# Performance work log

Measured on AMD Instinct MI355X. Metric: run time of the kernel, lower is better.

The kernel has to match this reference:

```python
import jax, jax.numpy as jnp
import numpy as np

B, T, N = 8, 128, 512
HID = 4              # hidden_channels (GAT out, heads=1)
IN = 1               # in_channels (forced by unsqueeze(-1))
D = N * HID          # LSTM input == hidden size = 2048
E = 16384            # num edges (avg degree 32)
OUT = N              # out_channels
NEG_SLOPE = 0.2      # PyG GATConv default


def setup_inputs() -> dict:
    key = jax.random.key(0)
    ks = jax.random.split(key, 12)
    inv = 1.0 / np.sqrt(D)
    return {
        "x_sequence": jax.random.normal(ks[0], (B, T, N), jnp.float32),
        "gat_w": jax.random.normal(ks[1], (HID, IN), jnp.float32),
        "att_src": jax.random.normal(ks[2], (HID,), jnp.float32) * 0.5,
        "att_dst": jax.random.normal(ks[3], (HID,), jnp.float32) * 0.5,
        "gat_bias": jnp.zeros((HID,), jnp.float32),
        "w_ih": jax.random.normal(ks[4], (4 * D, D), jnp.float32) * inv,
        "w_hh": jax.random.normal(ks[5], (4 * D, D), jnp.float32) * inv,
        "b_ih": jnp.zeros((4 * D,), jnp.float32),
        "b_hh": jnp.zeros((4 * D,), jnp.float32),
        "w_lin": jax.random.normal(ks[6], (OUT, D), jnp.float32) * inv,
        "b_lin": jnp.zeros((OUT,), jnp.float32),
        "edge_index": jax.random.randint(ks[7], (2, E), 0, N, jnp.int32),
    }


def _gat(x_flat, src, dst, W, a_s, a_d, bias):
    # x_flat: [BN, 1]; PyG GATConv heads=1, eval mode (dropout off)
    BN = B * N
    h = x_flat @ W.T                                   # [BN, HID]
    e = jax.nn.leaky_relu((h @ a_s)[src] + (h @ a_d)[dst], NEG_SLOPE)
    m = jax.ops.segment_max(e, dst, num_segments=BN)   # every node has a self-loop
    ex = jnp.exp(e - m[dst])
    denom = jax.ops.segment_sum(ex, dst, num_segments=BN)
    alpha = ex / denom[dst]
    out = jax.ops.segment_sum(alpha[:, None] * h[src], dst, num_segments=BN)
    return out + bias


def reference(x_sequence, gat_w, att_src, att_dst, gat_bias,
              w_ih, w_hh, b_ih, b_hh, w_lin, b_lin, edge_index):
    BN = B * N
    # add self-loops over all B*N flattened nodes (PyG add_self_loops=True);
    # original edge_index only touches nodes < N -- faithfully reproduced.
    loops = jnp.arange(BN, dtype=edge_index.dtype)
    src = jnp.concatenate([edge_index[0], loops])
    dst = jnp.concatenate([edge_index[1], loops])

    # batch the per-timestep GAT: [T, B*N, 1]
    xt = x_sequence.transpose(1, 0, 2).reshape(T, BN, IN)
    g = jax.vmap(lambda x: jax.nn.relu(
        _gat(x, src, dst, gat_w, att_src, att_dst, gat_bias)))(xt)  # [T, BN, HID]
    seq = g.reshape(T, B, D)                           # [T, B, N*HID]

    def step(carry, x_t):
        h, c = carry
        z = x_t @ w_ih.T + h @ w_hh.T + (b_ih + b_hh)  # [B, 4D]
        i, f, gg, o = jnp.split(z, 4, axis=-1)         # torch gate order i,f,g,o
        c = jax.nn.sigmoid(f) * c + jax.nn.sigmoid(i) * jnp.tanh(gg)
        h = jax.nn.sigmoid(o) * jnp.tanh(c)
        return (h, c), None

    h0 = jnp.zeros((B, D), x_sequence.dtype)
    (hT, _), _ = jax.lax.scan(step, (h0, h0), seq)     # hT == lstm_out[:, -1, :]
    return hT @ w_lin.T + b_lin                        # [B, OUT]
```

## Files before the change

kernel.cpp:

```cpp
#include <hip/hip_runtime.h>
#include <hip/hip_cooperative_groups.h>
#include <math.h>

#define BB 8
#define TT 128
#define NN 512
#define HH 4
#define DD 2048
#define EE 16384
#define KTOT 4096
#define NKB 128
#define XROW 4112
#define FPAD 16

typedef __attribute__((ext_vector_type(8))) short short8;
typedef __attribute__((ext_vector_type(4))) float f32x4;

__device__ __forceinline__ float b2f(unsigned short u) {
    union { unsigned int i; float f; } v; v.i = ((unsigned int)u) << 16; return v.f;
}
__device__ __forceinline__ unsigned short f2b(float f) {
    union { float f; unsigned int i; } v; v.f = f;
    unsigned int r = v.i + 0x7fff + ((v.i >> 16) & 1);
    return (unsigned short)(r >> 16);
}


__global__ void k_csr_zero(int* __restrict__ counts, int* __restrict__ fill) {
    int i = threadIdx.x;
    counts[i] = 0;
    fill[i] = 0;
}

__global__ void k_csr_count(const int* __restrict__ ei, int* __restrict__ counts) {
    int e = blockIdx.x * blockDim.x + threadIdx.x;
    if (e < EE) atomicAdd(&counts[ei[EE + e]], 1);
}

__global__ void k_csr_scan(const int* __restrict__ counts, int* __restrict__ offs) {
    int s = 0;
    for (int i = 0; i < NN; ++i) { offs[i] = s; s += counts[i]; }
    offs[NN] = s;
}

__global__ void k_csr_fill(const int* __restrict__ ei, const int* __restrict__ offs,
                           int* __restrict__ fill, int* __restrict__ csr_src) {
    int e = blockIdx.x * blockDim.x + threadIdx.x;
    if (e < EE) {
        int d = ei[EE + e];
        int pos = atomicAdd(&fill[d], 1);
        csr_src[offs[d] + pos] = ei[e];
    }
}


__global__ void k_gat0(const float* __restrict__ xseq, const float* __restrict__ W,
                       const float* __restrict__ as, const float* __restrict__ ad,
                       const float* __restrict__ bias, const int* __restrict__ offs,
                       const int* __restrict__ csr_src, unsigned short* __restrict__ seqout) {
    __shared__ float xr[NN];
    const int t = blockIdx.x;
    const int j = threadIdx.x;
    xr[j] = xseq[t * NN + j];
    __syncthreads();

    const float w0 = W[0], w1 = W[1], w2 = W[2], w3 = W[3];
    const float cs = w0 * as[0] + w1 * as[1] + w2 * as[2] + w3 * as[3];
    const float cd = w0 * ad[0] + w1 * ad[1] + w2 * ad[2] + w3 * ad[3];

    const float xj = xr[j];
    const float ed = cd * xj;
    float e0 = (cs + cd) * xj;
    e0 = e0 > 0.f ? e0 : 0.2f * e0;

    const int s0 = offs[j], s1 = offs[j + 1];
    float m = e0;
    for (int p = s0; p < s1; ++p) {
        float e = cs * xr[csr_src[p]] + ed;
        e = e > 0.f ? e : 0.2f * e;
        m = fmaxf(m, e);
    }
    float den = expf(e0 - m);
    float num = den * xj;
    for (int p = s0; p < s1; ++p) {
        int s = csr_src[p];
        float e = cs * xr[s] + ed;
        e = e > 0.f ? e : 0.2f * e;
        float wgt = expf(e - m);
        den += wgt;
        num += wgt * xr[s];
    }
    const float y = num / den;

    ushort4 o;
    o.x = f2b(fmaxf(w0 * y + bias[0], 0.f));
    o.y = f2b(fmaxf(w1 * y + bias[1], 0.f));
    o.z = f2b(fmaxf(w2 * y + bias[2], 0.f));
    o.w = f2b(fmaxf(w3 * y + bias[3], 0.f));
    *(ushort4*)(seqout + (size_t)t * BB * DD + (size_t)j * HH) = o;
}

__global__ void k_gat_rest(const float* __restrict__ xseq, const float* __restrict__ W,
                           const float* __restrict__ bias, unsigned short* __restrict__ seqout) {
    int n = blockIdx.x * blockDim.x + threadIdx.x;
    int t = n / (7 * NN);
    int rem = n - t * (7 * NN);
    int b = 1 + rem / NN;
    int j = rem - (b - 1) * NN;
    float x = xseq[((size_t)b * TT + t) * NN + j];
    const float w0 = W[0], w1 = W[1], w2 = W[2], w3 = W[3];
    ushort4 o;
    o.x = f2b(fmaxf(w0 * x + bias[0], 0.f));
    o.y = f2b(fmaxf(w1 * x + bias[1], 0.f));
    o.z = f2b(fmaxf(w2 * x + bias[2], 0.f));
    o.w = f2b(fmaxf(w3 * x + bias[3], 0.f));
    *(ushort4*)(seqout + (size_t)t * BB * DD + (size_t)b * DD + (size_t)j * HH) = o;
}

__global__ __launch_bounds__(256) void k_pack_w(const float* __restrict__ wih,
                                                const float* __restrict__ whh,
                                                unsigned short* __restrict__ WP) {
    const int pair = blockIdx.x * 4 + (threadIdx.x >> 6);
    const int lane = threadIdx.x & 63;
    const int s = pair >> 7, kb = pair & 127;
    const int n = lane >> 2, quad = lane & 3;
    const int d = (s >> 1) * 8 + (s & 1) * 4 + (n & 3);
    const int row = (n >> 2) * 2048 + d;
    const int k = kb * 32 + quad * 8;
    const float* src = (k < 2048) ? (wih + (size_t)row * 2048 + k)
                                  : (whh + (size_t)row * 2048 + (k - 2048));
    unsigned int u[4];
#pragma unroll
    for (int p = 0; p < 4; ++p)
        u[p] = (unsigned int)f2b(src[2 * p]) | ((unsigned int)f2b(src[2 * p + 1]) << 16);
    ((uint4*)WP)[(size_t)pair * 64 + quad * 16 + n] = make_uint4(u[0], u[1], u[2], u[3]);
}


__global__ void k_zero(unsigned int* __restrict__ hb, unsigned int* __restrict__ bar) {
    int i = blockIdx.x * blockDim.x + threadIdx.x;
    if (i < 16384) hb[i] = 0u;
    if (i < 256 * FPAD) bar[i] = 0u;
}

__global__ __launch_bounds__(1024, 4) void k_lstm_persist(
    const unsigned short* __restrict__ seq, const uint4* __restrict__ WPq,
    const float* __restrict__ b_ih, const float* __restrict__ b_hh,
    unsigned short* __restrict__ hb0, unsigned short* __restrict__ hb1,
    unsigned int* __restrict__ flags) {
    __shared__ unsigned short xh[8][XROW];
    __shared__ float red[2][8][32][4];
    __shared__ float zbuf[4][8][8];
    __shared__ float biasL[32];

    const int tid = threadIdx.x;
    const int wave = tid >> 6, lane = tid & 63;
    const int st = wave >> 3, ke = wave & 7;
    const int d0 = blockIdx.x * 8;
    const size_t sglob = (size_t)blockIdx.x * 2 + st;

    if (tid < 32) {
        const int g = tid >> 3, dl = tid & 7;
        const int row = g * 2048 + d0 + dl;
        biasL[tid] = b_ih[row] + b_hh[row];
    }

    uint4 w[16];
    {
        const uint4* wp = WPq + (sglob * NKB + (size_t)ke * 16) * 64 + lane;
#pragma unroll
        for (int i = 0; i < 16; ++i) w[i] = wp[i * 64];
    }

    const unsigned short* arow = &xh[lane & 7][(lane >> 4) << 3];

    float creg0 = 0.f, creg1 = 0.f;

    for (int t = 0; t < TT; ++t) {
        const unsigned short* xt = seq + (size_t)t * BB * DD;
        const unsigned short* hin = (t & 1) ? hb1 : hb0;
        unsigned short* hout = (t & 1) ? hb0 : hb1;

#pragma unroll
        for (int i = 0; i < 2; ++i) {
            const int c = tid + 1024 * i;
            const int batch = c >> 8;
            const int k = (c & 255) << 3;
            *(uint4*)&xh[batch][k] = *(const uint4*)(xt + batch * DD + k);
        }

        if (t > 0 && tid < 256) {
            const unsigned int gen = (unsigned int)t;
            while (__hip_atomic_load(&flags[tid * FPAD], __ATOMIC_RELAXED,
                                     __HIP_MEMORY_SCOPE_AGENT) < gen) {}
        }
        __syncthreads();

        const unsigned int* hw = (const unsigned int*)hin;
#pragma unroll
        for (int i = 0; i < 8; ++i) {
            const int widx = tid + 1024 * i;
            const int batch = widx >> 10;
            const int dw = widx & 1023;
            unsigned int v = __hip_atomic_load(&hw[widx], __ATOMIC_RELAXED,
                                               __HIP_MEMORY_SCOPE_AGENT);
            ((unsigned int*)&xh[batch][2048])[dw] = v;
        }
        __syncthreads();

        f32x4 acc = {0.f, 0.f, 0.f, 0.f};
#pragma unroll
        for (int i = 0; i < 16; ++i) {
            const int kb = ke * 16 + i;
            short8 a = *(const short8*)(arow + (kb << 5));
            short8 b;
            __builtin_memcpy(&b, &w[i], 16);
            acc = __builtin_amdgcn_mfma_f32_16x16x32_bf16(a, b, acc, 0, 0, 0);
        }
        if (lane < 32) *(f32x4*)&red[st][ke][lane][0] = acc;
        __syncthreads();

        if (tid < 256) {
            const int st2 = tid >> 7, l2 = (tid & 127) >> 2, reg = tid & 3;
            float z = 0.f;
#pragma unroll
            for (int kk = 0; kk < 8; ++kk) z += red[st2][kk][l2][reg];
            const int batch = (l2 >> 4) * 4 + reg;
            const int n = l2 & 15;
            zbuf[n >> 2][st2 * 4 + (n & 3)][batch] = z;
        }
        __syncthreads();

        if (tid < 32) {
            const int batch = tid >> 2, dp = (tid & 3) << 1;
            float h2[2];
#pragma unroll
            for (int q = 0; q < 2; ++q) {
                const int dl = dp + q;
                const float zi = zbuf[0][dl][batch] + biasL[dl];
                const float zf = zbuf[1][dl][batch] + biasL[8 + dl];
                const float zg = zbuf[2][dl][batch] + biasL[16 + dl];
                const float zo = zbuf[3][dl][batch] + biasL[24 + dl];
                const float si = 1.f / (1.f + expf(-zi));
                const float sf = 1.f / (1.f + expf(-zf));
                const float so = 1.f / (1.f + expf(-zo));
                const float tg = tanhf(zg);
                float& cr = q ? creg1 : creg0;
                cr = sf * cr + si * tg;
                h2[q] = so * tanhf(cr);
            }
            const unsigned int pk = (unsigned int)f2b(h2[0]) |
                                    ((unsigned int)f2b(h2[1]) << 16);
            unsigned int* hp = (unsigned int*)(hout + batch * DD + d0) + (tid & 3);
            __hip_atomic_store(hp, pk, __ATOMIC_RELAXED, __HIP_MEMORY_SCOPE_AGENT);
        }
        if (t != TT - 1) {
            __builtin_amdgcn_s_waitcnt(0);
            if (tid == 0)
                __hip_atomic_store(&flags[blockIdx.x * FPAD], (unsigned int)(t + 1),
                                   __ATOMIC_RELAXED, __HIP_MEMORY_SCOPE_AGENT);
        }
    }
}

__global__ void k_final(const unsigned short* __restrict__ h, const float* __restrict__ w_lin,
                        const float* __restrict__ b_lin, float* __restrict__ out) {
    const int wave = threadIdx.x >> 6;
    const int lane = threadIdx.x & 63;
    const int o = blockIdx.x * 4 + wave;
    const float4* w4 = (const float4*)(w_lin + (size_t)o * DD);

    float acc[8];
#pragma unroll
    for (int b = 0; b < 8; ++b) acc[b] = 0.f;
#pragma unroll 2
    for (int it = 0; it < 8; ++it) {
        const int k4 = it * 64 + lane;
        float4 wv = w4[k4];
#pragma unroll
        for (int b = 0; b < 8; ++b) {
            ushort4 hv = *(const ushort4*)(h + (size_t)b * DD + 4 * (size_t)k4);
            acc[b] += wv.x * b2f(hv.x) + wv.y * b2f(hv.y) +
                      wv.z * b2f(hv.z) + wv.w * b2f(hv.w);
        }
    }
#pragma unroll
    for (int b = 0; b < 8; ++b) {
        float v = acc[b];
        v += __shfl_xor(v, 32, 64);
        v += __shfl_xor(v, 16, 64);
        v += __shfl_xor(v, 8, 64);
        v += __shfl_xor(v, 4, 64);
        v += __shfl_xor(v, 2, 64);
        v += __shfl_xor(v, 1, 64);
        acc[b] = v;
    }
    if (lane < 8) out[(size_t)lane * NN + o] = acc[lane] + b_lin[o];
}


extern "C" void kernel_launch(void* const* d_in, const int* in_sizes, int n_in,
                              void* d_out, int out_size, void* d_ws, size_t ws_size,
                              hipStream_t stream) {
    const float* xseq  = (const float*)d_in[0];
    const float* gat_w = (const float*)d_in[1];
    const float* a_src = (const float*)d_in[2];
    const float* a_dst = (const float*)d_in[3];
    const float* g_b   = (const float*)d_in[4];
    const float* w_ih  = (const float*)d_in[5];
    const float* w_hh  = (const float*)d_in[6];
    const float* b_ih  = (const float*)d_in[7];
    const float* b_hh  = (const float*)d_in[8];
    const float* w_lin = (const float*)d_in[9];
    const float* b_lin = (const float*)d_in[10];
    const int*   eidx  = (const int*)d_in[11];
    float* out = (float*)d_out;

    unsigned short* seq = (unsigned short*)d_ws;
    unsigned short* WP  = seq + (size_t)TT * BB * DD;
    unsigned short* hb0 = WP + (size_t)8192 * KTOT;
    unsigned short* hb1 = hb0 + BB * DD;
    unsigned int* flags = (unsigned int*)(hb1 + BB * DD);
    int* counts  = (int*)(flags + 256 * FPAD);
    int* offs    = counts + NN;
    int* fill    = offs + NN + 1;
    int* csr_src = fill + NN;

    k_csr_zero<<<1, NN, 0, stream>>>(counts, fill);
    k_csr_count<<<EE / 256, 256, 0, stream>>>(eidx, counts);
    k_csr_scan<<<1, 1, 0, stream>>>(counts, offs);
    k_csr_fill<<<EE / 256, 256, 0, stream>>>(eidx, offs, fill, csr_src);

    k_pack_w<<<16384, 256, 0, stream>>>(w_ih, w_hh, WP);

    k_gat0<<<TT, NN, 0, stream>>>(xseq, gat_w, a_src, a_dst, g_b, offs, csr_src, seq);
    k_gat_rest<<<(TT * 7 * NN) / 256, 256, 0, stream>>>(xseq, gat_w, g_b, seq);

    k_zero<<<64, 256, 0, stream>>>((unsigned int*)hb0, flags);

    {
        void* kargs[] = {
            (void*)&seq, (void*)&WP, (void*)&b_ih, (void*)&b_hh,
            (void*)&hb0, (void*)&hb1, (void*)&flags,
        };
        hipLaunchCooperativeKernel((const void*)k_lstm_persist, dim3(256), dim3(1024),
                                   kargs, 0, stream);
    }

    k_final<<<NN / 4, 256, 0, stream>>>(hb0, w_lin, b_lin, out);
}
```

Measured before the change: 964.5 us.

## Fuse GAT into one atomic-scatter kernel and load LSTM operands straight to registers

The CSR build kernels and the two GAT kernels are replaced by one kernel per timestep. It scatters edge softmax numerators and denominators with shared-memory atomics and skips the max subtraction, then writes all batches. In the persistent LSTM kernel the x and h operands are now loaded directly from global memory into registers instead of being staged in LDS. The x-part MFMAs are issued before the flag wait, which removes a barrier and lets input work overlap the cross-block sync. The weight packer also switches to float4 loads. Dropping the max subtraction risks overflow in expf for large logits.

```diff
diff --git a/kernel.cpp b/kernel.cpp
--- a/kernel.cpp
+++ b/kernel.cpp
@@ -1,16 +1,13 @@
 #include <hip/hip_runtime.h>
-#include <hip/hip_cooperative_groups.h>
 #include <math.h>
 
 #define BB 8
 #define TT 128
 #define NN 512
-#define HH 4
 #define DD 2048
 #define EE 16384
 #define KTOT 4096
 #define NKB 128
-#define XROW 4112
 #define FPAD 16
 
 typedef __attribute__((ext_vector_type(8))) short short8;
@@ -25,96 +22,60 @@
     return (unsigned short)(r >> 16);
 }
 
-
-__global__ void k_csr_zero(int* __restrict__ counts, int* __restrict__ fill) {
-    int i = threadIdx.x;
-    counts[i] = 0;
-    fill[i] = 0;
-}
-
-__global__ void k_csr_count(const int* __restrict__ ei, int* __restrict__ counts) {
-    int e = blockIdx.x * blockDim.x + threadIdx.x;
-    if (e < EE) atomicAdd(&counts[ei[EE + e]], 1);
-}
-
-__global__ void k_csr_scan(const int* __restrict__ counts, int* __restrict__ offs) {
-    int s = 0;
-    for (int i = 0; i < NN; ++i) { offs[i] = s; s += counts[i]; }
-    offs[NN] = s;
-}
-
-__global__ void k_csr_fill(const int* __restrict__ ei, const int* __restrict__ offs,
-                           int* __restrict__ fill, int* __restrict__ csr_src) {
-    int e = blockIdx.x * blockDim.x + threadIdx.x;
-    if (e < EE) {
-        int d = ei[EE + e];
-        int pos = atomicAdd(&fill[d], 1);
-        csr_src[offs[d] + pos] = ei[e];
-    }
-}
-
-
-__global__ void k_gat0(const float* __restrict__ xseq, const float* __restrict__ W,
-                       const float* __restrict__ as, const float* __restrict__ ad,
-                       const float* __restrict__ bias, const int* __restrict__ offs,
-                       const int* __restrict__ csr_src, unsigned short* __restrict__ seqout) {
-    __shared__ float xr[NN];
+__global__ __launch_bounds__(512) void k_gat(const float* __restrict__ xseq,
+                                             const float* __restrict__ W,
+                                             const float* __restrict__ as,
+                                             const float* __restrict__ ad,
+                                             const float* __restrict__ bias,
+                                             const int* __restrict__ ei,
+                                             unsigned short* __restrict__ seqout) {
+    __shared__ float xr[NN], num[NN], den[NN];
     const int t = blockIdx.x;
     const int j = threadIdx.x;
     xr[j] = xseq[t * NN + j];
-    __syncthreads();
+    num[j] = 0.f;
+    den[j] = 0.f;
 
     const float w0 = W[0], w1 = W[1], w2 = W[2], w3 = W[3];
     const float cs = w0 * as[0] + w1 * as[1] + w2 * as[2] + w3 * as[3];
     const float cd = w0 * ad[0] + w1 * ad[1] + w2 * ad[2] + w3 * ad[3];
-
-    const float xj = xr[j];
-    const float ed = cd * xj;
-    float e0 = (cs + cd) * xj;
-    e0 = e0 > 0.f ? e0 : 0.2f * e0;
-
-    const int s0 = offs[j], s1 = offs[j + 1];
-    float m = e0;
-    for (int p = s0; p < s1; ++p) {
-        float e = cs * xr[csr_src[p]] + ed;
-        e = e > 0.f ? e : 0.2f * e;
-        m = fmaxf(m, e);
-    }
-    float den = expf(e0 - m);
-    float num = den * xj;
-    for (int p = s0; p < s1; ++p) {
-        int s = csr_src[p];
-        float e = cs * xr[s] + ed;
-        e = e > 0.f ? e : 0.2f * e;
-        float wgt = expf(e - m);
-        den += wgt;
-        num += wgt * xr[s];
-    }
-    const float y = num / den;
-
-    ushort4 o;
-    o.x = f2b(fmaxf(w0 * y + bias[0], 0.f));
-    o.y = f2b(fmaxf(w1 * y + bias[1], 0.f));
-    o.z = f2b(fmaxf(w2 * y + bias[2], 0.f));
-    o.w = f2b(fmaxf(w3 * y + bias[3], 0.f));
-    *(ushort4*)(seqout + (size_t)t * BB * DD + (size_t)j * HH) = o;
-}
-
-__global__ void k_gat_rest(const float* __restrict__ xseq, const float* __restrict__ W,
-                           const float* __restrict__ bias, unsigned short* __restrict__ seqout) {
-    int n = blockIdx.x * blockDim.x + threadIdx.x;
-    int t = n / (7 * NN);
-    int rem = n - t * (7 * NN);
-    int b = 1 + rem / NN;
-    int j = rem - (b - 1) * NN;
-    float x = xseq[((size_t)b * TT + t) * NN + j];
-    const float w0 = W[0], w1 = W[1], w2 = W[2], w3 = W[3];
-    ushort4 o;
-    o.x = f2b(fmaxf(w0 * x + bias[0], 0.f));
-    o.y = f2b(fmaxf(w1 * x + bias[1], 0.f));
-    o.z = f2b(fmaxf(w2 * x + bias[2], 0.f));
-    o.w = f2b(fmaxf(w3 * x + bias[3], 0.f));
-    *(ushort4*)(seqout + (size_t)t * BB * DD + (size_t)b * DD + (size_t)j * HH) = o;
+    __syncthreads();
+
+    for (int e = j; e < EE; e += NN) {
+        const int s = ei[e], d = ei[EE + e];
+        float v = cs * xr[s] + cd * xr[d];
+        v = v > 0.f ? v : 0.2f * v;
+        const float wt = expf(v);
+        atomicAdd(&den[d], wt);
+        atomicAdd(&num[d], wt * xr[s]);
+    }
+    __syncthreads();
+
+    const float b0 = bias[0], b1 = bias[1], b2 = bias[2], b3 = bias[3];
+
+    {
+        const float xj = xr[j];
+        float e0 = (cs + cd) * xj;
+        e0 = e0 > 0.f ? e0 : 0.2f * e0;
+        const float we = expf(e0);
+        const float y = (num[j] + we * xj) / (den[j] + we);
+        ushort4 o;
+        o.x = f2b(fmaxf(w0 * y + b0, 0.f));
+        o.y = f2b(fmaxf(w1 * y + b1, 0.f));
+        o.z = f2b(fmaxf(w2 * y + b2, 0.f));
+        o.w = f2b(fmaxf(w3 * y + b3, 0.f));
+        *(ushort4*)(seqout + (size_t)t * BB * DD + (size_t)j * 4) = o;
+    }
+#pragma unroll
+    for (int b = 1; b < 8; ++b) {
+        const float x = xseq[((size_t)b * TT + t) * NN + j];
+        ushort4 o;
+        o.x = f2b(fmaxf(w0 * x + b0, 0.f));
+        o.y = f2b(fmaxf(w1 * x + b1, 0.f));
+        o.z = f2b(fmaxf(w2 * x + b2, 0.f));
+        o.w = f2b(fmaxf(w3 * x + b3, 0.f));
+        *(ushort4*)(seqout + (size_t)t * BB * DD + (size_t)b * DD + (size_t)j * 4) = o;
+    }
 }
 
 __global__ __launch_bounds__(256) void k_pack_w(const float* __restrict__ wih,
@@ -129,11 +90,13 @@
     const int k = kb * 32 + quad * 8;
     const float* src = (k < 2048) ? (wih + (size_t)row * 2048 + k)
                                   : (whh + (size_t)row * 2048 + (k - 2048));
-    unsigned int u[4];
-#pragma unroll
-    for (int p = 0; p < 4; ++p)
-        u[p] = (unsigned int)f2b(src[2 * p]) | ((unsigned int)f2b(src[2 * p + 1]) << 16);
-    ((uint4*)WP)[(size_t)pair * 64 + quad * 16 + n] = make_uint4(u[0], u[1], u[2], u[3]);
+    const float4 f0 = ((const float4*)src)[0];
+    const float4 f1 = ((const float4*)src)[1];
+    unsigned int u0 = (unsigned int)f2b(f0.x) | ((unsigned int)f2b(f0.y) << 16);
+    unsigned int u1 = (unsigned int)f2b(f0.z) | ((unsigned int)f2b(f0.w) << 16);
+    unsigned int u2 = (unsigned int)f2b(f1.x) | ((unsigned int)f2b(f1.y) << 16);
+    unsigned int u3 = (unsigned int)f2b(f1.z) | ((unsigned int)f2b(f1.w) << 16);
+    ((uint4*)WP)[(size_t)pair * 64 + quad * 16 + n] = make_uint4(u0, u1, u2, u3);
 }
 
 
@@ -148,7 +111,6 @@
     const float* __restrict__ b_ih, const float* __restrict__ b_hh,
     unsigned short* __restrict__ hb0, unsigned short* __restrict__ hb1,
     unsigned int* __restrict__ flags) {
-    __shared__ unsigned short xh[8][XROW];
     __shared__ float red[2][8][32][4];
     __shared__ float zbuf[4][8][8];
     __shared__ float biasL[32];
@@ -167,12 +129,19 @@
 
     uint4 w[16];
     {
-        const uint4* wp = WPq + (sglob * NKB + (size_t)ke * 16) * 64 + lane;
-#pragma unroll
-        for (int i = 0; i < 16; ++i) w[i] = wp[i * 64];
-    }
-
-    const unsigned short* arow = &xh[lane & 7][(lane >> 4) << 3];
+        const uint4* wpx = WPq + (sglob * NKB + (size_t)ke * 8) * 64 + lane;
+        const uint4* wph = WPq + (sglob * NKB + 64 + (size_t)ke * 8) * 64 + lane;
+#pragma unroll
+        for (int i = 0; i < 8; ++i) {
+            w[i] = wpx[i * 64];
+            w[8 + i] = wph[i * 64];
+        }
+    }
+
+    const int batch = lane & 7;
+    const int quad = lane >> 4;
+    const int xoff = batch * DD + ke * 256 + quad * 8;
+    const int hqoff = batch * 512 + ke * 64 + quad * 2;
 
     float creg0 = 0.f, creg1 = 0.f;
 
@@ -181,12 +150,20 @@
         const unsigned short* hin = (t & 1) ? hb1 : hb0;
         unsigned short* hout = (t & 1) ? hb0 : hb1;
 
-#pragma unroll
-        for (int i = 0; i < 2; ++i) {
-            const int c = tid + 1024 * i;
-            const int batch = c >> 8;
-            const int k = (c & 255) << 3;
-            *(uint4*)&xh[batch][k] = *(const uint4*)(xt + batch * DD + k);
+        f32x4 c0 = {0.f, 0.f, 0.f, 0.f}, c1 = {0.f, 0.f, 0.f, 0.f};
+        {
+            uint4 ax[8];
+#pragma unroll
+            for (int i = 0; i < 8; ++i)
+                ax[i] = *(const uint4*)(xt + xoff + i * 32);
+#pragma unroll
+            for (int i = 0; i < 8; ++i) {
+                short8 a, b;
+                __builtin_memcpy(&a, &ax[i], 16);
+                __builtin_memcpy(&b, &w[i], 16);
+                if (i & 1) c1 = __builtin_amdgcn_mfma_f32_16x16x32_bf16(a, b, c1, 0, 0, 0);
+                else       c0 = __builtin_amdgcn_mfma_f32_16x16x32_bf16(a, b, c0, 0, 0, 0);
+            }
         }
 
         if (t > 0 && tid < 256) {
@@ -196,27 +173,26 @@
         }
         __syncthreads();
 
-        const unsigned int* hw = (const unsigned int*)hin;
-#pragma unroll
-        for (int i = 0; i < 8; ++i) {
-            const int widx = tid + 1024 * i;
-            const int batch = widx >> 10;
-            const int dw = widx & 1023;
-            unsigned int v = __hip_atomic_load(&hw[widx], __ATOMIC_RELAXED,
-                                               __HIP_MEMORY_SCOPE_AGENT);
-            ((unsigned int*)&xh[batch][2048])[dw] = v;
-        }
-        __syncthreads();
-
-        f32x4 acc = {0.f, 0.f, 0.f, 0.f};
-#pragma unroll
-        for (int i = 0; i < 16; ++i) {
-            const int kb = ke * 16 + i;
-            short8 a = *(const short8*)(arow + (kb << 5));
-            short8 b;
-            __builtin_memcpy(&b, &w[i], 16);
-            acc = __builtin_amdgcn_mfma_f32_16x16x32_bf16(a, b, acc, 0, 0, 0);
-        }
+        {
+            const unsigned long long* hq = (const unsigned long long*)hin;
+            unsigned long long ah[8][2];
+#pragma unroll
+            for (int i = 0; i < 8; ++i) {
+                ah[i][0] = __hip_atomic_load(&hq[hqoff + i * 8], __ATOMIC_RELAXED,
+                                             __HIP_MEMORY_SCOPE_AGENT);
+                ah[i][1] = __hip_atomic_load(&hq[hqoff + i * 8 + 1], __ATOMIC_RELAXED,
+                                             __HIP_MEMORY_SCOPE_AGENT);
+            }
+#pragma unroll
+            for (int i = 0; i < 8; ++i) {
+                short8 a, b;
+                __builtin_memcpy(&a, &ah[i][0], 16);
+                __builtin_memcpy(&b, &w[8 + i], 16);
+                if (i & 1) c1 = __builtin_amdgcn_mfma_f32_16x16x32_bf16(a, b, c1, 0, 0, 0);
+                else       c0 = __builtin_amdgcn_mfma_f32_16x16x32_bf16(a, b, c0, 0, 0, 0);
+            }
+        }
+        f32x4 acc = c0 + c1;
         if (lane < 32) *(f32x4*)&red[st][ke][lane][0] = acc;
         __syncthreads();
 
@@ -225,22 +201,22 @@
             float z = 0.f;
 #pragma unroll
             for (int kk = 0; kk < 8; ++kk) z += red[st2][kk][l2][reg];
-            const int batch = (l2 >> 4) * 4 + reg;
+            const int bb = (l2 >> 4) * 4 + reg;
             const int n = l2 & 15;
-            zbuf[n >> 2][st2 * 4 + (n & 3)][batch] = z;
+            zbuf[n >> 2][st2 * 4 + (n & 3)][bb] = z;
         }
         __syncthreads();
 
         if (tid < 32) {
-            const int batch = tid >> 2, dp = (tid & 3) << 1;
+            const int bb = tid >> 2, dp = (tid & 3) << 1;
             float h2[2];
 #pragma unroll
             for (int q = 0; q < 2; ++q) {
                 const int dl = dp + q;
-                const float zi = zbuf[0][dl][batch] + biasL[dl];
-                const float zf = zbuf[1][dl][batch] + biasL[8 + dl];
-                const float zg = zbuf[2][dl][batch] + biasL[16 + dl];
-                const float zo = zbuf[3][dl][batch] + biasL[24 + dl];
+                const float zi = zbuf[0][dl][bb] + biasL[dl];
+                const float zf = zbuf[1][dl][bb] + biasL[8 + dl];
+                const float zg = zbuf[2][dl][bb] + biasL[16 + dl];
+                const float zo = zbuf[3][dl][bb] + biasL[24 + dl];
                 const float si = 1.f / (1.f + expf(-zi));
                 const float sf = 1.f / (1.f + expf(-zf));
                 const float so = 1.f / (1.f + expf(-zo));
@@ -251,7 +227,7 @@
             }
             const unsigned int pk = (unsigned int)f2b(h2[0]) |
                                     ((unsigned int)f2b(h2[1]) << 16);
-            unsigned int* hp = (unsigned int*)(hout + batch * DD + d0) + (tid & 3);
+            unsigned int* hp = (unsigned int*)(hout + bb * DD + d0) + (tid & 3);
             __hip_atomic_store(hp, pk, __ATOMIC_RELAXED, __HIP_MEMORY_SCOPE_AGENT);
         }
         if (t != TT - 1) {
@@ -321,20 +297,10 @@
     unsigned short* hb0 = WP + (size_t)8192 * KTOT;
     unsigned short* hb1 = hb0 + BB * DD;
     unsigned int* flags = (unsigned int*)(hb1 + BB * DD);
-    int* counts  = (int*)(flags + 256 * FPAD);
-    int* offs    = counts + NN;
-    int* fill    = offs + NN + 1;
-    int* csr_src = fill + NN;
-
-    k_csr_zero<<<1, NN, 0, stream>>>(counts, fill);
-    k_csr_count<<<EE / 256, 256, 0, stream>>>(eidx, counts);
-    k_csr_scan<<<1, 1, 0, stream>>>(counts, offs);
-    k_csr_fill<<<EE / 256, 256, 0, stream>>>(eidx, offs, fill, csr_src);
 
     k_pack_w<<<16384, 256, 0, stream>>>(w_ih, w_hh, WP);
 
-    k_gat0<<<TT, NN, 0, stream>>>(xseq, gat_w, a_src, a_dst, g_b, offs, csr_src, seq);
-    k_gat_rest<<<(TT * 7 * NN) / 256, 256, 0, stream>>>(xseq, gat_w, g_b, seq);
+    k_gat<<<TT, NN, 0, stream>>>(xseq, gat_w, a_src, a_dst, g_b, eidx, seq);
 
     k_zero<<<64, 256, 0, stream>>>((unsigned int*)hb0, flags);
 
```

New measurement: 1.762 ms. 1.83x slower.
